# Optimization experiments

Measured on AMD Instinct MI355X. Metric: run time of the kernel, lower is better.

## Reference

```python
import jax, jax.numpy as jnp
import numpy as np

N_NODES = 10000
N_EDGES = 640000
IN_FEAT = 128
HIDDEN = 128
CLASSES = 2
NEG_SLOPE = 0.2


def glorot(key, shape):
    lim = float(np.sqrt(6.0 / (shape[0] + shape[-1])))
    return jax.random.uniform(key, shape, jnp.float32, -lim, lim)


def setup_inputs() -> dict:
    key = jax.random.key(0)
    ks = jax.random.split(key, 10)
    x = jax.random.normal(ks[0], (N_NODES, IN_FEAT), jnp.float32)
    edge_index = jax.random.randint(ks[1], (2, N_EDGES), 0, N_NODES, jnp.int64)
    return {
        "x": x,
        "edge_index": edge_index,
        "W1": glorot(ks[2], (IN_FEAT, HIDDEN)),
        "a_src1": glorot(ks[3], (HIDDEN, 1))[:, 0],
        "a_dst1": glorot(ks[4], (HIDDEN, 1))[:, 0],
        "b1": jnp.zeros((HIDDEN,), jnp.float32),
        "W2": glorot(ks[5], (HIDDEN, CLASSES)),
        "a_src2": glorot(ks[6], (CLASSES, 1))[:, 0],
        "a_dst2": glorot(ks[7], (CLASSES, 1))[:, 0],
        "b2": jnp.zeros((CLASSES,), jnp.float32),
    }


def gat_conv(x, src, dst, W, a_src, a_dst, b, n_nodes):
    # x: [N, Fin] -> h: [N, Fout]
    h = x @ W
    # per-node attention logits (single head)
    alpha_s = h @ a_src  # [N]
    alpha_d = h @ a_dst  # [N]
    e = jax.nn.leaky_relu(alpha_s[src] + alpha_d[dst], NEG_SLOPE)  # [E]
    # segment softmax over incoming edges of each dst node
    m = jax.ops.segment_max(e, dst, num_segments=n_nodes)
    ex = jnp.exp(e - m[dst])
    denom = jax.ops.segment_sum(ex, dst, num_segments=n_nodes)
    w = ex / denom[dst]  # [E]
    # weighted scatter-aggregate of source messages
    out = jax.ops.segment_sum(h[src] * w[:, None], dst, num_segments=n_nodes)
    return out + b


def reference(x, edge_index, W1, a_src1, a_dst1, b1, W2, a_src2, a_dst2, b2):
    n = x.shape[0]
    # PyG GATConv default: add self-loops
    loops = jnp.arange(n, dtype=edge_index.dtype)
    src = jnp.concatenate([edge_index[0], loops])
    dst = jnp.concatenate([edge_index[1], loops])
    h = gat_conv(x, src, dst, W1, a_src1, a_dst1, b1, n)
    h = jax.nn.relu(h)
    out = gat_conv(h, src, dst, W2, a_src2, a_dst2, b2, n)
    return out
```

## Files before the change

### kernel.cpp

```cpp
#include <hip/hip_runtime.h>
#include <hip/hip_bf16.h>

#define NN 10000
#define NE 640000
#define ETOT (NE + NN)
#define FEAT 128
#define NEG 0.2f
#define CAP 160
#define NBUCK 157
#define EPB 4096
#define NB1 ((ETOT + EPB - 1) / EPB)
#define JSLOT 96
#define GEMM_ROWS 16
#define NBG (NN / GEMM_ROWS)
#define NJOB1 (NB1 + NBG)
#define NJAGG ((NN + 3) / 4)

typedef short bf16x8 __attribute__((ext_vector_type(8)));
typedef float f32x4  __attribute__((ext_vector_type(4)));

__device__ __forceinline__ short f2bf(float f) {
    unsigned u = __float_as_uint(f);
    unsigned r = (u + 0x7FFFu + ((u >> 16) & 1u)) >> 16;
    return (short)r;
}

union ShMem {
    struct {
        int hist[160]; int scan[256]; int excl[160]; int cursor[160];
        unsigned int pairs[EPB];
    } p;
    struct { float wal[FEAT]; float wdl[FEAT]; } g;
};

__device__ __forceinline__ int detect64(const void* ep) {
    const unsigned long long* p64 = (const unsigned long long*)ep;
    unsigned long long v = p64[threadIdx.x & 63];
    unsigned long long bal = __ballot((v >> 32) != 0ULL);
    return (bal == 0ULL) ? 1 : 0;
}

__device__ __forceinline__ void bin_job(const void* ep, int flag64,
        unsigned int* __restrict__ staged, int* __restrict__ jcnt,
        ShMem& sh, int tid, int job) {
    for (int i = tid; i < 160; i += 256) sh.p.hist[i] = 0;
    __syncthreads();
    const int e0 = job * EPB;
    int nE = ETOT - e0; if (nE > EPB) nE = EPB;
    const bool full = (nE == EPB);
    unsigned int key[16];
    if (full) {
#pragma unroll
        for (int k = 0; k < 16; k++) {
            int e = e0 + tid + k * 256, s, d;
            if (e < NE) {
                if (flag64) { const long long* p = (const long long*)ep; s = (int)p[e]; d = (int)p[NE + e]; }
                else        { const int* p = (const int*)ep;       s = p[e];       d = p[NE + e]; }
            } else { s = e - NE; d = s; }
            key[k] = ((unsigned)d << 14) | (unsigned)s;
            atomicAdd(&sh.p.hist[d >> 6], 1);
        }
    } else {
        for (int k = 0; k < 16; k++) {
            int idx = tid + k * 256;
            if (idx < nE) {
                int e = e0 + idx, s, d;
                if (e < NE) {
                    if (flag64) { const long long* p = (const long long*)ep; s = (int)p[e]; d = (int)p[NE + e]; }
                    else        { const int* p = (const int*)ep;       s = p[e];       d = p[NE + e]; }
                } else { s = e - NE; d = s; }
                atomicAdd(&sh.p.hist[d >> 6], 1);
            }
        }
    }
    __syncthreads();
    sh.p.scan[tid] = (tid < 160) ? sh.p.hist[tid] : 0;
    __syncthreads();
    for (int off = 1; off < 256; off <<= 1) {
        int t = (tid >= off) ? sh.p.scan[tid - off] : 0;
        __syncthreads();
        sh.p.scan[tid] += t;
        __syncthreads();
    }
    if (tid < 160) {
        int ex = sh.p.scan[tid] - sh.p.hist[tid];
        sh.p.excl[tid] = ex;
        sh.p.cursor[tid] = ex;
        if (tid < NBUCK) jcnt[tid * NB1 + job] = min(sh.p.hist[tid], JSLOT);
    }
    __syncthreads();
    if (full) {
#pragma unroll
        for (int k = 0; k < 16; k++) {
            int b = key[k] >> 20;
            int pos = atomicAdd(&sh.p.cursor[b], 1);
            sh.p.pairs[pos] = key[k];
        }
    } else {
        for (int k = 0; k < 16; k++) {
            int idx = tid + k * 256;
            if (idx < nE) {
                int e = e0 + idx, s, d;
                if (e < NE) {
                    if (flag64) { const long long* p = (const long long*)ep; s = (int)p[e]; d = (int)p[NE + e]; }
                    else        { const int* p = (const int*)ep;       s = p[e];       d = p[NE + e]; }
                } else { s = e - NE; d = s; }
                unsigned int kk = ((unsigned)d << 14) | (unsigned)s;
                int pos = atomicAdd(&sh.p.cursor[d >> 6], 1);
                sh.p.pairs[pos] = kk;
            }
        }
    }
    __syncthreads();
    for (int i = tid; i < nE; i += 256) {
        unsigned int kk = sh.p.pairs[i];
        int b = kk >> 20;
        int pos = i - sh.p.excl[b];
        if (pos < JSLOT) staged[(size_t)(b * NB1 + job) * JSLOT + pos] = kk;
    }
}

__device__ __forceinline__ void gemm_job(
        const float* __restrict__ x, const float* __restrict__ W1,
        const float* __restrict__ a_src1, const float* __restrict__ a_dst1,
        unsigned short* __restrict__ h1, float* __restrict__ as1, float* __restrict__ ad1,
        ShMem& sh, int tid, int gb) {
    const int row0 = gb * GEMM_ROWS;
    const int lane = tid & 63, wv = tid >> 6;
    const int m = lane & 15, g = lane >> 4;
    const int n0 = wv * 32;

    {
        int jj = tid & 127;
        const float* wrow = W1 + (size_t)jj * FEAT;
        const float* avec = (tid < 128) ? a_src1 : a_dst1;
        float acc = 0.f;
        for (int k = 0; k < FEAT; k++) acc += wrow[k] * avec[k];
        if (tid < 128) sh.g.wal[jj] = acc; else sh.g.wdl[jj] = acc;
    }
    __syncthreads();

    const float* arow = x + (size_t)(row0 + m) * FEAT + g * 8;
    const float* w1c0 = W1 + n0 + m;
    const float* w1c1 = W1 + n0 + 16 + m;
    const bool do_logit = (wv == 0);
    f32x4 acc0 = {0.f, 0.f, 0.f, 0.f}, acc1 = {0.f, 0.f, 0.f, 0.f};
    float la = 0.f, ld = 0.f;
#pragma unroll
    for (int kt = 0; kt < 4; kt++) {
        float4 v0 = *(const float4*)(arow + kt * 32);
        float4 v1 = *(const float4*)(arow + kt * 32 + 4);
        if (do_logit) {
            const float* wap = sh.g.wal + g * 8 + kt * 32;
            const float* wdp = sh.g.wdl + g * 8 + kt * 32;
            la += v0.x * wap[0] + v0.y * wap[1] + v0.z * wap[2] + v0.w * wap[3]
                + v1.x * wap[4] + v1.y * wap[5] + v1.z * wap[6] + v1.w * wap[7];
            ld += v0.x * wdp[0] + v0.y * wdp[1] + v0.z * wdp[2] + v0.w * wdp[3]
                + v1.x * wdp[4] + v1.y * wdp[5] + v1.z * wdp[6] + v1.w * wdp[7];
        }
        bf16x8 a;
        a[0] = f2bf(v0.x); a[1] = f2bf(v0.y); a[2] = f2bf(v0.z); a[3] = f2bf(v0.w);
        a[4] = f2bf(v1.x); a[5] = f2bf(v1.y); a[6] = f2bf(v1.z); a[7] = f2bf(v1.w);
        bf16x8 b0, b1;
#pragma unroll
        for (int i = 0; i < 8; i++) {
            int k = kt * 32 + g * 8 + i;
            b0[i] = f2bf(w1c0[(size_t)k * FEAT]);
            b1[i] = f2bf(w1c1[(size_t)k * FEAT]);
        }
        acc0 = __builtin_amdgcn_mfma_f32_16x16x32_bf16(a, b0, acc0, 0, 0, 0);
        acc1 = __builtin_amdgcn_mfma_f32_16x16x32_bf16(a, b1, acc1, 0, 0, 0);
    }
    if (do_logit) {
        la += __shfl_xor(la, 16); la += __shfl_xor(la, 32);
        ld += __shfl_xor(ld, 16); ld += __shfl_xor(ld, 32);
        if (g == 0) { as1[row0 + m] = la; ad1[row0 + m] = ld; }
    }
#pragma unroll
    for (int r = 0; r < 4; r++) {
        int row = row0 + g * 4 + r;
        h1[(size_t)row * FEAT + n0 + m]      = (unsigned short)f2bf(acc0[r]);
        h1[(size_t)row * FEAT + n0 + 16 + m] = (unsigned short)f2bf(acc1[r]);
    }
}

__global__ __launch_bounds__(256) void fat1_kernel(const void* ep,
        const float* __restrict__ x, const float* __restrict__ W1,
        const float* __restrict__ a_src1, const float* __restrict__ a_dst1,
        unsigned int* __restrict__ staged, int* __restrict__ jcnt,
        unsigned short* __restrict__ h1, float* __restrict__ as1, float* __restrict__ ad1) {
    __shared__ ShMem sh;
    int blk = blockIdx.x, tid = threadIdx.x;
    if (blk < NB1) { int f = detect64(ep); bin_job(ep, f, staged, jcnt, sh, tid, blk); }
    else gemm_job(x, W1, a_src1, a_dst1, h1, as1, ad1, sh, tid, blk - NB1);
}

__global__ __launch_bounds__(1024) void scatter2_kernel(const int* __restrict__ jcnt,
        const unsigned int* __restrict__ staged, int* __restrict__ slots, int* __restrict__ deg) {
    __shared__ int cnt_s[NB1];
    __shared__ int ncnt[64];
    int b = blockIdx.x, tid = threadIdx.x;
    if (tid < 64) ncnt[tid] = 0;
    for (int j = tid; j < NB1; j += 1024) cnt_s[j] = jcnt[b * NB1 + j];
    __syncthreads();
    int wv = tid >> 6, lane = tid & 63;
    for (int j = wv; j < NB1; j += 16) {
        int c = cnt_s[j];
        const unsigned int* seg = staged + (size_t)(b * NB1 + j) * JSLOT;
        for (int i = lane; i < c; i += 64) {
            unsigned int kk = seg[i];
            int d = kk >> 14, s = kk & 0x3FFF;
            int lp = atomicAdd(&ncnt[d & 63], 1);
            if (lp < CAP) slots[d * CAP + lp] = s;
        }
    }
    __syncthreads();
    if (tid < 64) {
        int node = b * 64 + tid;
        if (node < NN) deg[node] = min(ncnt[tid], CAP);
    }
}

__global__ __launch_bounds__(256) void agg1_kernel(const int* __restrict__ deg,
        const int* __restrict__ slots, const float* __restrict__ as1,
        const float* __restrict__ ad1, const unsigned int* __restrict__ h1u,
        const float* __restrict__ b1, const float* __restrict__ W2,
        const float* __restrict__ a_src2, const float* __restrict__ a_dst2,
        float* __restrict__ h2, float* __restrict__ as2, float* __restrict__ ad2) {
    __shared__ float2 ws_s[4][CAP];
    int tid = threadIdx.x;
    int wi = tid >> 6, lane = tid & 63;
    int v = blockIdx.x * 4 + wi;
    if (v >= NN) return;
    int c = deg[v];
    const int base = v * CAP;
    float adv = ad1[v];

    int i0 = lane, i1 = lane + 64, i2 = lane + 128;
    float dsum = 0.f;
    if (i0 < c) {
        int s = slots[base + i0];
        float t = as1[s] + adv; t = (t > 0.f) ? t : NEG * t;
        float w = __expf(fminf(t, 80.f));
        ws_s[wi][i0] = make_float2(w, __int_as_float(s)); dsum += w;
    }
    if (i1 < c) {
        int s = slots[base + i1];
        float t = as1[s] + adv; t = (t > 0.f) ? t : NEG * t;
        float w = __expf(fminf(t, 80.f));
        ws_s[wi][i1] = make_float2(w, __int_as_float(s)); dsum += w;
    }
    if (i2 < c) {
        int s = slots[base + i2];
        float t = as1[s] + adv; t = (t > 0.f) ? t : NEG * t;
        float w = __expf(fminf(t, 80.f));
        ws_s[wi][i2] = make_float2(w, __int_as_float(s)); dsum += w;
    }
#pragma unroll
    for (int o = 32; o; o >>= 1) dsum += __shfl_xor(dsum, o);

    float ax = 0.f, ay = 0.f;
#pragma unroll 4
    for (int i = 0; i < c; i++) {
        float2 ws = ws_s[wi][i];
        float wgt = ws.x;
        int s = __float_as_int(ws.y);
        unsigned int u = h1u[s * 64 + lane];
        ax += wgt * __uint_as_float(u << 16);
        ay += wgt * __uint_as_float(u & 0xFFFF0000u);
    }
    float inv = 1.f / dsum;
    float2 bb = ((const float2*)b1)[lane];
    float hx = fmaxf(ax * inv + bb.x, 0.f);
    float hy = fmaxf(ay * inv + bb.y, 0.f);

    const float2* w2p = (const float2*)W2;
    float2 wc0 = w2p[2 * lane], wc1 = w2p[2 * lane + 1];
    float c0 = hx * wc0.x + hy * wc1.x;
    float c1 = hx * wc0.y + hy * wc1.y;
#pragma unroll
    for (int o = 32; o; o >>= 1) { c0 += __shfl_down(c0, o); c1 += __shfl_down(c1, o); }
    if (lane == 0) {
        ((float2*)h2)[v] = make_float2(c0, c1);
        as2[v] = c0 * a_src2[0] + c1 * a_src2[1];
        ad2[v] = c0 * a_dst2[0] + c1 * a_dst2[1];
    }
}

__global__ __launch_bounds__(256) void agg2_kernel(const int* __restrict__ deg,
        const int* __restrict__ slots, const float* __restrict__ as2,
        const float* __restrict__ ad2, const float* __restrict__ h2,
        const float* __restrict__ b2, float* __restrict__ out) {
    int tid = threadIdx.x;
    int wi = tid >> 6, lane = tid & 63;
    int v = blockIdx.x * 4 + wi;
    if (v >= NN) return;
    int c = deg[v];
    int base = v * CAP;
    float adv = ad2[v];
    float dsum = 0.f, a0 = 0.f, a1 = 0.f;
    for (int i = lane; i < c; i += 64) {
        int s = slots[base + i];
        float e = as2[s] + adv;
        e = (e > 0.f) ? e : NEG * e;
        float w = __expf(fminf(e, 80.f));
        dsum += w;
        float2 hv = ((const float2*)h2)[s];
        a0 += w * hv.x; a1 += w * hv.y;
    }
#pragma unroll
    for (int o = 32; o; o >>= 1) {
        dsum += __shfl_xor(dsum, o);
        a0 += __shfl_xor(a0, o);
        a1 += __shfl_xor(a1, o);
    }
    if (lane == 0) {
        out[v * 2]     = a0 / dsum + b2[0];
        out[v * 2 + 1] = a1 / dsum + b2[1];
    }
}

extern "C" void kernel_launch(void* const* d_in, const int* in_sizes, int n_in,
                              void* d_out, int out_size, void* d_ws, size_t ws_size,
                              hipStream_t stream) {
    const float* x      = (const float*)d_in[0];
    const void*  edges  = d_in[1];
    const float* W1     = (const float*)d_in[2];
    const float* a_src1 = (const float*)d_in[3];
    const float* a_dst1 = (const float*)d_in[4];
    const float* b1     = (const float*)d_in[5];
    const float* W2     = (const float*)d_in[6];
    const float* a_src2 = (const float*)d_in[7];
    const float* a_dst2 = (const float*)d_in[8];
    const float* b2     = (const float*)d_in[9];
    float* out = (float*)d_out;

    char* w = (char*)d_ws;
    size_t off = 0;
    auto alloc = [&](size_t bytes) { void* p = w + off; off += (bytes + 255) & ~size_t(255); return p; };
    unsigned int*    staged = (unsigned int*)alloc((size_t)NBUCK * NB1 * JSLOT * 4);
    int*             jcnt   = (int*)alloc((size_t)NBUCK * NB1 * 4);
    int*             slots  = (int*)alloc((size_t)NN * CAP * 4);
    int*             deg    = (int*)alloc((size_t)NN * 4);
    unsigned short*  h1     = (unsigned short*)alloc((size_t)NN * FEAT * 2);
    float*           as1    = (float*)alloc(NN * 4);
    float*           ad1    = (float*)alloc(NN * 4);
    float*           h2     = (float*)alloc(NN * 2 * 4);
    float*           as2    = (float*)alloc(NN * 4);
    float*           ad2    = (float*)alloc(NN * 4);

    fat1_kernel<<<NJOB1, 256, 0, stream>>>(edges, x, W1, a_src1, a_dst1,
                                           staged, jcnt, h1, as1, ad1);
    scatter2_kernel<<<NBUCK, 1024, 0, stream>>>(jcnt, staged, slots, deg);
    agg1_kernel<<<NJAGG, 256, 0, stream>>>(deg, slots, as1, ad1,
                                           (const unsigned int*)h1, b1,
                                           W2, a_src2, a_dst2, h2, as2, ad2);
    agg2_kernel<<<NJAGG, 256, 0, stream>>>(deg, slots, as2, ad2, h2, b2, out);
}
```

Measured before the change: 60.06 us.

## Fuse scatter and layer-1 aggregation into one kernel with per-bucket flags

Merges the scatter kernel and the first aggregation kernel into a single launch. The first 157 blocks bin edges into per-node slots and then set a per-bucket ready flag. The remaining blocks spin on their bucket's flag before aggregating, so aggregation can start as soon as its bucket is ready and one launch boundary is removed. The scatter blocks drop from 1024 to 256 threads, which cuts scatter parallelism. Correctness relies on scatter blocks being scheduled before or alongside the spinning blocks, so forward progress rests on block dispatch order.

```diff
diff --git a/kernel.cpp b/kernel.cpp
--- a/kernel.cpp
+++ b/kernel.cpp
@@ -33,6 +33,11 @@
     struct { float wal[FEAT]; float wdl[FEAT]; } g;
 };
 
+union ShMem2 {
+    struct { int cnt_s[NB1]; int ncnt[64]; } s;
+    struct { float2 ws[4][CAP]; } a;
+};
+
 __device__ __forceinline__ int detect64(const void* ep) {
     const unsigned long long* p64 = (const unsigned long long*)ep;
     unsigned long long v = p64[threadIdx.x & 63];
@@ -129,7 +134,6 @@
     const int lane = tid & 63, wv = tid >> 6;
     const int m = lane & 15, g = lane >> 4;
     const int n0 = wv * 32;
-
     {
         int jj = tid & 127;
         const float* wrow = W1 + (size_t)jj * FEAT;
@@ -188,50 +192,60 @@
         const float* __restrict__ x, const float* __restrict__ W1,
         const float* __restrict__ a_src1, const float* __restrict__ a_dst1,
         unsigned int* __restrict__ staged, int* __restrict__ jcnt,
-        unsigned short* __restrict__ h1, float* __restrict__ as1, float* __restrict__ ad1) {
+        unsigned short* __restrict__ h1, float* __restrict__ as1, float* __restrict__ ad1,
+        int* __restrict__ bflag) {
     __shared__ ShMem sh;
     int blk = blockIdx.x, tid = threadIdx.x;
+    if (blk < NBUCK && tid == 0) bflag[blk] = 0;
     if (blk < NB1) { int f = detect64(ep); bin_job(ep, f, staged, jcnt, sh, tid, blk); }
     else gemm_job(x, W1, a_src1, a_dst1, h1, as1, ad1, sh, tid, blk - NB1);
 }
 
-__global__ __launch_bounds__(1024) void scatter2_kernel(const int* __restrict__ jcnt,
-        const unsigned int* __restrict__ staged, int* __restrict__ slots, int* __restrict__ deg) {
-    __shared__ int cnt_s[NB1];
-    __shared__ int ncnt[64];
-    int b = blockIdx.x, tid = threadIdx.x;
-    if (tid < 64) ncnt[tid] = 0;
-    for (int j = tid; j < NB1; j += 1024) cnt_s[j] = jcnt[b * NB1 + j];
-    __syncthreads();
-    int wv = tid >> 6, lane = tid & 63;
-    for (int j = wv; j < NB1; j += 16) {
-        int c = cnt_s[j];
-        const unsigned int* seg = staged + (size_t)(b * NB1 + j) * JSLOT;
-        for (int i = lane; i < c; i += 64) {
-            unsigned int kk = seg[i];
-            int d = kk >> 14, s = kk & 0x3FFF;
-            int lp = atomicAdd(&ncnt[d & 63], 1);
-            if (lp < CAP) slots[d * CAP + lp] = s;
-        }
-    }
-    __syncthreads();
-    if (tid < 64) {
-        int node = b * 64 + tid;
-        if (node < NN) deg[node] = min(ncnt[tid], CAP);
-    }
-}
-
-__global__ __launch_bounds__(256) void agg1_kernel(const int* __restrict__ deg,
-        const int* __restrict__ slots, const float* __restrict__ as1,
-        const float* __restrict__ ad1, const unsigned int* __restrict__ h1u,
+__global__ __launch_bounds__(256) void scatagg_kernel(const int* __restrict__ jcnt,
+        const unsigned int* __restrict__ staged, int* __restrict__ slots,
+        int* __restrict__ deg, int* __restrict__ bflag,
+        const float* __restrict__ as1, const float* __restrict__ ad1,
+        const unsigned int* __restrict__ h1u,
         const float* __restrict__ b1, const float* __restrict__ W2,
         const float* __restrict__ a_src2, const float* __restrict__ a_dst2,
         float* __restrict__ h2, float* __restrict__ as2, float* __restrict__ ad2) {
-    __shared__ float2 ws_s[4][CAP];
+    __shared__ ShMem2 sh;
     int tid = threadIdx.x;
+    if (blockIdx.x < NBUCK) {
+        int b = blockIdx.x;
+        if (tid < 64) sh.s.ncnt[tid] = 0;
+        for (int j = tid; j < NB1; j += 256) sh.s.cnt_s[j] = jcnt[b * NB1 + j];
+        __syncthreads();
+        int wv = tid >> 6, lane = tid & 63;
+        for (int j = wv; j < NB1; j += 4) {
+            int c = sh.s.cnt_s[j];
+            const unsigned int* seg = staged + (size_t)(b * NB1 + j) * JSLOT;
+            for (int i = lane; i < c; i += 64) {
+                unsigned int kk = seg[i];
+                int d = kk >> 14, s = kk & 0x3FFF;
+                int lp = atomicAdd(&sh.s.ncnt[d & 63], 1);
+                if (lp < CAP) slots[d * CAP + lp] = s;
+            }
+        }
+        __syncthreads();
+        if (tid < 64) {
+            int node = b * 64 + tid;
+            if (node < NN) deg[node] = min(sh.s.ncnt[tid], CAP);
+        }
+        __threadfence();
+        __syncthreads();
+        if (tid == 0) atomicExch(&bflag[b], 1);
+        return;
+    }
+    int j = blockIdx.x - NBUCK;
+    int b = j >> 4;
+    if (tid == 0) {
+        while (atomicAdd(&bflag[b], 0) == 0) __builtin_amdgcn_s_sleep(8);
+    }
+    __syncthreads();
+
     int wi = tid >> 6, lane = tid & 63;
-    int v = blockIdx.x * 4 + wi;
-    if (v >= NN) return;
+    int v = j * 4 + wi;
     int c = deg[v];
     const int base = v * CAP;
     float adv = ad1[v];
@@ -242,19 +256,19 @@
         int s = slots[base + i0];
         float t = as1[s] + adv; t = (t > 0.f) ? t : NEG * t;
         float w = __expf(fminf(t, 80.f));
-        ws_s[wi][i0] = make_float2(w, __int_as_float(s)); dsum += w;
+        sh.a.ws[wi][i0] = make_float2(w, __int_as_float(s)); dsum += w;
     }
     if (i1 < c) {
         int s = slots[base + i1];
         float t = as1[s] + adv; t = (t > 0.f) ? t : NEG * t;
         float w = __expf(fminf(t, 80.f));
-        ws_s[wi][i1] = make_float2(w, __int_as_float(s)); dsum += w;
+        sh.a.ws[wi][i1] = make_float2(w, __int_as_float(s)); dsum += w;
     }
     if (i2 < c) {
         int s = slots[base + i2];
         float t = as1[s] + adv; t = (t > 0.f) ? t : NEG * t;
         float w = __expf(fminf(t, 80.f));
-        ws_s[wi][i2] = make_float2(w, __int_as_float(s)); dsum += w;
+        sh.a.ws[wi][i2] = make_float2(w, __int_as_float(s)); dsum += w;
     }
 #pragma unroll
     for (int o = 32; o; o >>= 1) dsum += __shfl_xor(dsum, o);
@@ -262,7 +276,7 @@
     float ax = 0.f, ay = 0.f;
 #pragma unroll 4
     for (int i = 0; i < c; i++) {
-        float2 ws = ws_s[wi][i];
+        float2 ws = sh.a.ws[wi][i];
         float wgt = ws.x;
         int s = __float_as_int(ws.y);
         unsigned int u = h1u[s * 64 + lane];
@@ -342,6 +356,7 @@
     int*             jcnt   = (int*)alloc((size_t)NBUCK * NB1 * 4);
     int*             slots  = (int*)alloc((size_t)NN * CAP * 4);
     int*             deg    = (int*)alloc((size_t)NN * 4);
+    int*             bflag  = (int*)alloc((size_t)NBUCK * 4);
     unsigned short*  h1     = (unsigned short*)alloc((size_t)NN * FEAT * 2);
     float*           as1    = (float*)alloc(NN * 4);
     float*           ad1    = (float*)alloc(NN * 4);
@@ -350,10 +365,10 @@
     float*           ad2    = (float*)alloc(NN * 4);
 
     fat1_kernel<<<NJOB1, 256, 0, stream>>>(edges, x, W1, a_src1, a_dst1,
-                                           staged, jcnt, h1, as1, ad1);
-    scatter2_kernel<<<NBUCK, 1024, 0, stream>>>(jcnt, staged, slots, deg);
-    agg1_kernel<<<NJAGG, 256, 0, stream>>>(deg, slots, as1, ad1,
-                                           (const unsigned int*)h1, b1,
-                                           W2, a_src2, a_dst2, h2, as2, ad2);
+                                           staged, jcnt, h1, as1, ad1, bflag);
+    scatagg_kernel<<<NBUCK + NJAGG, 256, 0, stream>>>(jcnt, staged, slots, deg, bflag,
+                                                      as1, ad1, (const unsigned int*)h1,
+                                                      b1, W2, a_src2, a_dst2,
+                                                      h2, as2, ad2);
     agg2_kernel<<<NJAGG, 256, 0, stream>>>(deg, slots, as2, ad2, h2, b2, out);
 }
```

New measurement: 87.28 us. 45.3% more time.
